# Optimization experiments

Hardware: AMD Instinct MI355X
Metric: run time of the kernel (lower is better)

## Reference

```python
import jax, jax.numpy as jnp
import numpy as np

HEADS = 4
K = 3  # neighborhood kernel size
EPS = 1e-5


def _nbr_idx(dim, k):
    # NATTEN semantics: window start clamped so the full k-window stays in-bounds.
    i = jnp.arange(dim)
    start = jnp.clip(i - k // 2, 0, dim - k)
    return start[:, None] + jnp.arange(k)[None, :]  # [dim, k]


def _gather_windows(t, ix, iy, iz):
    # t: [B, X, Y, Z, n, c] -> [B, X, Y, Z, K^3, n, c]
    t = t[:, ix]                 # [B, X, k, Y, Z, n, c]
    t = t[:, :, :, iy]           # [B, X, k, Y, k, Z, n, c]
    t = t[:, :, :, :, :, iz]     # [B, X, k, Y, k, Z, k, n, c]
    t = t.transpose(0, 1, 3, 5, 2, 4, 6, 7, 8)  # [B,X,Y,Z,k,k,k,n,c]
    B, X, Y, Z = t.shape[0], t.shape[1], t.shape[2], t.shape[3]
    return t.reshape(B, X, Y, Z, K * K * K, HEADS, -1)


def setup_inputs() -> dict:
    key = jax.random.key(0)
    k1, k2, k3 = jax.random.split(key, 3)
    C = 128
    x = jax.random.normal(k1, (1, C, 32, 32, 32), dtype=jnp.float32)
    ln_gamma = jnp.ones((C,), jnp.float32)
    ln_beta = jnp.zeros((C,), jnp.float32)
    qkv_w = jax.random.normal(k2, (3 * C, C), dtype=jnp.float32) * 0.02
    qkv_b = jnp.zeros((3 * C,), jnp.float32)
    proj_w = jax.random.normal(k3, (C, C), dtype=jnp.float32) * 0.02
    proj_b = jnp.zeros((C,), jnp.float32)
    return {"x": x, "ln_gamma": ln_gamma, "ln_beta": ln_beta,
            "qkv_w": qkv_w, "qkv_b": qkv_b, "proj_w": proj_w, "proj_b": proj_b}


def reference(x, ln_gamma, ln_beta, qkv_w, qkv_b, proj_w, proj_b):
    B, C, X, Y, Z = x.shape
    hd = C // HEADS
    scale = hd ** -0.5

    # permute to channels-last + LayerNorm over C
    h = x.transpose(0, 2, 3, 4, 1)  # [B,X,Y,Z,C]
    mu = jnp.mean(h, axis=-1, keepdims=True)
    var = jnp.mean(jnp.square(h - mu), axis=-1, keepdims=True)
    h = (h - mu) * jax.lax.rsqrt(var + EPS) * ln_gamma + ln_beta

    # QKV projection
    qkv = h @ qkv_w.T + qkv_b                     # [B,X,Y,Z,3C]
    q, k, v = jnp.split(qkv, 3, axis=-1)
    q = q.reshape(B, X, Y, Z, HEADS, hd)
    k = k.reshape(B, X, Y, Z, HEADS, hd)
    v = v.reshape(B, X, Y, Z, HEADS, hd)

    ix, iy, iz = _nbr_idx(X, K), _nbr_idx(Y, K), _nbr_idx(Z, K)
    k_win = _gather_windows(k, ix, iy, iz)  # [B,X,Y,Z,27,n,hd]
    v_win = _gather_windows(v, ix, iy, iz)

    attn = jnp.einsum('bxyznc,bxyzknc->bxyznk', q * scale, k_win)
    attn = jax.nn.softmax(attn, axis=-1)
    out = jnp.einsum('bxyznk,bxyzknc->bxyznc', attn, v_win)
    out = out.reshape(B, X, Y, Z, C)

    out = out @ proj_w.T + proj_b                 # output projection
    return out.transpose(0, 4, 1, 2, 3) + x      # residual, channels-first
```

## Files before the change

### kernel.cpp

```cpp
#include <hip/hip_runtime.h>

#define N_VOX 32768
#define CCH 128
#define EPSV 1e-5f

typedef __attribute__((ext_vector_type(8))) short bfrag;
typedef __attribute__((ext_vector_type(4))) float ffrag;

__device__ __forceinline__ float bf2f(unsigned short u) {
    union { unsigned int i; float f; } c; c.i = ((unsigned int)u) << 16; return c.f;
}
__device__ __forceinline__ float bf2f_lo(unsigned int u) {
    union { unsigned int i; float f; } c; c.i = u << 16; return c.f;
}
__device__ __forceinline__ float bf2f_hi(unsigned int u) {
    union { unsigned int i; float f; } c; c.i = u & 0xFFFF0000u; return c.f;
}
__device__ __forceinline__ unsigned short f2bf(float f) {
    union { float f; unsigned int i; } c; c.f = f;
    unsigned int i = c.i;
    return (unsigned short)((i + 0x7FFFu + ((i >> 16) & 1u)) >> 16);
}

__global__ __launch_bounds__(256) void ln_kernel(const float* __restrict__ x,
                                                 const float* __restrict__ gamma,
                                                 const float* __restrict__ beta,
                                                 unsigned short* __restrict__ h) {
    __shared__ float xs[128 * 65];
    __shared__ float g[128], b[128];
    __shared__ float ps[256], pq[256];
    __shared__ float muS[64], rsS[64];
    int t = threadIdx.x;
    int v0 = blockIdx.x * 64;
    if (t < 128) { g[t] = gamma[t]; b[t] = beta[t]; }
    int vv = t & 63, cq = t >> 6;
    for (int cb = 0; cb < 32; cb++) {
        int c = cb * 4 + cq;
        xs[c * 65 + vv] = x[(size_t)c * N_VOX + v0 + vv];
    }
    __syncthreads();
    float s = 0.f, sq = 0.f;
    for (int i = 0; i < 32; i++) {
        float val = xs[(cq * 32 + i) * 65 + vv];
        s += val; sq += val * val;
    }
    ps[t] = s; pq[t] = sq;
    __syncthreads();
    if (t < 64) {
        float S = ps[t] + ps[t + 64] + ps[t + 128] + ps[t + 192];
        float Q = pq[t] + pq[t + 64] + pq[t + 128] + pq[t + 192];
        float mu = S * (1.0f / 128.0f);
        float var = Q * (1.0f / 128.0f) - mu * mu;
        muS[t] = mu; rsS[t] = rsqrtf(var + EPSV);
    }
    __syncthreads();
    int c8 = t & 15;
    for (int pass = 0; pass < 4; pass++) {
        int v = pass * 16 + (t >> 4);
        float mu = muS[v], rs = rsS[v];
        union { unsigned short u[8]; uint4 q; } pk;
        #pragma unroll
        for (int i = 0; i < 8; i++) {
            int c = c8 * 8 + i;
            float val = (xs[c * 65 + v] - mu) * rs * g[c] + b[c];
            pk.u[i] = f2bf(val);
        }
        *(uint4*)&h[(size_t)(v0 + v) * 128 + c8 * 8] = pk.q;
    }
}

__global__ __launch_bounds__(256) void qkv_gemm(const unsigned short* __restrict__ h,
                                                const float* __restrict__ w,
                                                const float* __restrict__ bias,
                                                unsigned short* __restrict__ qkv) {
    __shared__ __align__(16) unsigned short a_s[64 * 136];
    __shared__ __align__(16) unsigned short b_s[64 * 136];
    int t = threadIdx.x;
    int m0 = blockIdx.x * 64, o0 = blockIdx.y * 64;
    {
        int r4 = t >> 4, c8 = t & 15;
        #pragma unroll
        for (int pass = 0; pass < 4; pass++) {
            int r = pass * 16 + r4;
            *(uint4*)&a_s[r * 136 + c8 * 8] =
                *(const uint4*)&h[(size_t)(m0 + r) * 128 + c8 * 8];
            float4 w0 = *(const float4*)&w[(size_t)(o0 + r) * 128 + c8 * 8];
            float4 w1 = *(const float4*)&w[(size_t)(o0 + r) * 128 + c8 * 8 + 4];
            union { unsigned short u[8]; uint4 q; } pk;
            pk.u[0] = f2bf(w0.x); pk.u[1] = f2bf(w0.y);
            pk.u[2] = f2bf(w0.z); pk.u[3] = f2bf(w0.w);
            pk.u[4] = f2bf(w1.x); pk.u[5] = f2bf(w1.y);
            pk.u[6] = f2bf(w1.z); pk.u[7] = f2bf(w1.w);
            *(uint4*)&b_s[r * 136 + c8 * 8] = pk.q;
        }
    }
    __syncthreads();
    int wvi = t >> 6, lane = t & 63, m = lane & 15, quad = lane >> 4;
    ffrag acc[4] = {ffrag{0,0,0,0}, ffrag{0,0,0,0}, ffrag{0,0,0,0}, ffrag{0,0,0,0}};
    #pragma unroll
    for (int kk = 0; kk < 4; kk++) {
        bfrag a = *(bfrag*)&a_s[(wvi * 16 + m) * 136 + kk * 32 + quad * 8];
        #pragma unroll
        for (int nt = 0; nt < 4; nt++) {
            bfrag bb = *(bfrag*)&b_s[(nt * 16 + m) * 136 + kk * 32 + quad * 8];
            acc[nt] = __builtin_amdgcn_mfma_f32_16x16x32_bf16(a, bb, acc[nt], 0, 0, 0);
        }
    }
    #pragma unroll
    for (int nt = 0; nt < 4; nt++) {
        int o = o0 + nt * 16 + m;
        float bs = bias[o];
        int sec = o >> 7;
        int oc = o & 127;
        unsigned short* dst = qkv + (size_t)sec * ((size_t)N_VOX * 128);
        #pragma unroll
        for (int r = 0; r < 4; r++) {
            int vg = m0 + wvi * 16 + quad * 4 + r;
            dst[(size_t)vg * 128 + oc] = f2bf(acc[nt][r] + bs);
        }
    }
}

__global__ __launch_bounds__(256) void attn_kernel(const unsigned int* __restrict__ qb,
                                                   const unsigned int* __restrict__ kb,
                                                   const unsigned int* __restrict__ vb,
                                                   unsigned int* __restrict__ ob) {
    int t = threadIdx.x;
    int wave = t >> 6, lane = t & 63;
    int v = blockIdx.x * 4 + wave;
    int z = v & 31, y = (v >> 5) & 31, x = v >> 10;
    int sx = min(max(x - 1, 0), 29);
    int sy = min(max(y - 1, 0), 29);
    int sz = min(max(z - 1, 0), 29);
    int base = (sx << 10) + (sy << 5) + sz;
    const float scale = 0.17677669529663687f;
    unsigned int qpk = qb[(size_t)v * 64 + lane];
    float q0 = bf2f_lo(qpk) * scale;
    float q1 = bf2f_hi(qpk) * scale;
    float s[27];
    unsigned int vpk[27];
    #pragma unroll
    for (int j = 0; j < 27; j++) {
        int jx = j / 9, jy = (j % 9) / 3, jz = j % 3;
        int vj = base + (jx << 10) + (jy << 5) + jz;
        size_t idx = (size_t)vj * 64 + lane;
        unsigned int kpk = kb[idx];
        vpk[j] = vb[idx];
        float p = q0 * bf2f_lo(kpk) + q1 * bf2f_hi(kpk);
        p += __shfl_xor(p, 8);
        p += __shfl_xor(p, 4);
        p += __shfl_xor(p, 2);
        p += __shfl_xor(p, 1);
        s[j] = p;
    }
    float mx = s[0];
    #pragma unroll
    for (int j = 1; j < 27; j++) mx = fmaxf(mx, s[j]);
    float sum = 0.f;
    #pragma unroll
    for (int j = 0; j < 27; j++) { s[j] = __expf(s[j] - mx); sum += s[j]; }
    float inv = 1.0f / sum;
    float o0 = 0.f, o1 = 0.f;
    #pragma unroll
    for (int j = 0; j < 27; j++) {
        o0 += s[j] * bf2f_lo(vpk[j]);
        o1 += s[j] * bf2f_hi(vpk[j]);
    }
    unsigned int opk = ((unsigned int)f2bf(o0 * inv)) | (((unsigned int)f2bf(o1 * inv)) << 16);
    ob[(size_t)v * 64 + lane] = opk;
}

__global__ __launch_bounds__(256) void proj_gemm(const unsigned short* __restrict__ a,
                                                 const float* __restrict__ w,
                                                 const float* __restrict__ bias,
                                                 const float* __restrict__ xres,
                                                 float* __restrict__ out) {
    __shared__ __align__(16) unsigned short a_s[64 * 136];
    __shared__ __align__(16) unsigned short b_s[64 * 136];
    int t = threadIdx.x;
    int m0 = blockIdx.x * 64, o0 = blockIdx.y * 64;
    {
        int r4 = t >> 4, c8 = t & 15;
        #pragma unroll
        for (int pass = 0; pass < 4; pass++) {
            int r = pass * 16 + r4;
            *(uint4*)&a_s[r * 136 + c8 * 8] =
                *(const uint4*)&a[(size_t)(m0 + r) * 128 + c8 * 8];
            float4 w0 = *(const float4*)&w[(size_t)(o0 + r) * 128 + c8 * 8];
            float4 w1 = *(const float4*)&w[(size_t)(o0 + r) * 128 + c8 * 8 + 4];
            union { unsigned short u[8]; uint4 q; } pk;
            pk.u[0] = f2bf(w0.x); pk.u[1] = f2bf(w0.y);
            pk.u[2] = f2bf(w0.z); pk.u[3] = f2bf(w0.w);
            pk.u[4] = f2bf(w1.x); pk.u[5] = f2bf(w1.y);
            pk.u[6] = f2bf(w1.z); pk.u[7] = f2bf(w1.w);
            *(uint4*)&b_s[r * 136 + c8 * 8] = pk.q;
        }
    }
    __syncthreads();
    int wvi = t >> 6, lane = t & 63, m = lane & 15, quad = lane >> 4;
    ffrag acc[4] = {ffrag{0,0,0,0}, ffrag{0,0,0,0}, ffrag{0,0,0,0}, ffrag{0,0,0,0}};
    #pragma unroll
    for (int kk = 0; kk < 4; kk++) {
        bfrag av = *(bfrag*)&a_s[(wvi * 16 + m) * 136 + kk * 32 + quad * 8];
        #pragma unroll
        for (int nt = 0; nt < 4; nt++) {
            bfrag bb = *(bfrag*)&b_s[(nt * 16 + m) * 136 + kk * 32 + quad * 8];
            acc[nt] = __builtin_amdgcn_mfma_f32_16x16x32_bf16(av, bb, acc[nt], 0, 0, 0);
        }
    }
    #pragma unroll
    for (int nt = 0; nt < 4; nt++) {
        int o = o0 + nt * 16 + m;
        float bs = bias[o];
        int vg = m0 + wvi * 16 + quad * 4;
        float4 r = *(const float4*)&xres[(size_t)o * N_VOX + vg];
        float4 ov;
        ov.x = acc[nt][0] + bs + r.x;
        ov.y = acc[nt][1] + bs + r.y;
        ov.z = acc[nt][2] + bs + r.z;
        ov.w = acc[nt][3] + bs + r.w;
        *(float4*)&out[(size_t)o * N_VOX + vg] = ov;
    }
}

extern "C" void kernel_launch(void* const* d_in, const int* in_sizes, int n_in,
                              void* d_out, int out_size, void* d_ws, size_t ws_size,
                              hipStream_t stream) {
    const float* x      = (const float*)d_in[0];
    const float* gamma  = (const float*)d_in[1];
    const float* beta   = (const float*)d_in[2];
    const float* qkv_w  = (const float*)d_in[3];
    const float* qkv_b  = (const float*)d_in[4];
    const float* proj_w = (const float*)d_in[5];
    const float* proj_b = (const float*)d_in[6];
    float* out = (float*)d_out;

    unsigned short* h    = (unsigned short*)d_ws;
    unsigned short* qkv  = (unsigned short*)((char*)d_ws + (8u << 20));
    unsigned short* attn = h;

    hipLaunchKernelGGL(ln_kernel, dim3(512), dim3(256), 0, stream, x, gamma, beta, h);
    hipLaunchKernelGGL(qkv_gemm, dim3(512, 6), dim3(256), 0, stream, h, qkv_w, qkv_b, qkv);
    const unsigned short* qb = qkv;
    const unsigned short* kb = qkv + (size_t)N_VOX * 128;
    const unsigned short* vb = qkv + (size_t)2 * N_VOX * 128;
    hipLaunchKernelGGL(attn_kernel, dim3(8192), dim3(256), 0, stream,
                       (const unsigned int*)qb, (const unsigned int*)kb,
                       (const unsigned int*)vb, (unsigned int*)attn);
    hipLaunchKernelGGL(proj_gemm, dim3(512, 2), dim3(256), 0, stream, attn, proj_w, proj_b, x, out);
}
```

Before: 139.0 us.

## Fuse LayerNorm into QKV GEMM and pre-convert weights to bf16 once

LayerNorm output is now written directly into shared memory and reused by a single block that loops over all six QKV output tiles. This removes the global round trip of the normalized activations and the separate LN launch. A small kernel converts qkv_w and proj_w to bf16 once per call, so GEMM blocks no longer repeat the fp32-to-bf16 weight conversion. proj_gemm also loops over both output tiles per block, reusing the activation tile, and the attention output is written in place over q. The trade-off is far fewer blocks (512 instead of 3072 for QKV), more serialized work per block, and extra barriers, which may lower latency hiding.

```diff
diff --git a/kernel.cpp b/kernel.cpp
--- a/kernel.cpp
+++ b/kernel.cpp
@@ -7,9 +7,6 @@
 typedef __attribute__((ext_vector_type(8))) short bfrag;
 typedef __attribute__((ext_vector_type(4))) float ffrag;
 
-__device__ __forceinline__ float bf2f(unsigned short u) {
-    union { unsigned int i; float f; } c; c.i = ((unsigned int)u) << 16; return c.f;
-}
 __device__ __forceinline__ float bf2f_lo(unsigned int u) {
     union { unsigned int i; float f; } c; c.i = u << 16; return c.f;
 }
@@ -22,14 +19,39 @@
     return (unsigned short)((i + 0x7FFFu + ((i >> 16) & 1u)) >> 16);
 }
 
-__global__ __launch_bounds__(256) void ln_kernel(const float* __restrict__ x,
-                                                 const float* __restrict__ gamma,
-                                                 const float* __restrict__ beta,
-                                                 unsigned short* __restrict__ h) {
-    __shared__ float xs[128 * 65];
+__global__ __launch_bounds__(256) void convw_kernel(const float* __restrict__ qkv_w,
+                                                    const float* __restrict__ proj_w,
+                                                    unsigned short* __restrict__ wq,
+                                                    unsigned short* __restrict__ wp) {
+    int i = (blockIdx.x * 256 + threadIdx.x) * 4;
+    if (i < 384 * 128) {
+        float4 v = *(const float4*)&qkv_w[i];
+        ushort4 pk;
+        pk.x = f2bf(v.x); pk.y = f2bf(v.y); pk.z = f2bf(v.z); pk.w = f2bf(v.w);
+        *(ushort4*)&wq[i] = pk;
+    } else {
+        int j = i - 384 * 128;
+        float4 v = *(const float4*)&proj_w[j];
+        ushort4 pk;
+        pk.x = f2bf(v.x); pk.y = f2bf(v.y); pk.z = f2bf(v.z); pk.w = f2bf(v.w);
+        *(ushort4*)&wp[j] = pk;
+    }
+}
+
+__global__ __launch_bounds__(256) void ln_qkv_kernel(const float* __restrict__ x,
+                                                     const float* __restrict__ gamma,
+                                                     const float* __restrict__ beta,
+                                                     const unsigned short* __restrict__ wq,
+                                                     const float* __restrict__ bias,
+                                                     unsigned short* __restrict__ qkv) {
+    __shared__ __align__(16) unsigned short a_s[64 * 136];
+    __shared__ __align__(16) char pool[128 * 65 * 4];
     __shared__ float g[128], b[128];
     __shared__ float ps[256], pq[256];
     __shared__ float muS[64], rsS[64];
+    float* xs = (float*)pool;
+    unsigned short* b_s = (unsigned short*)pool;
+
     int t = threadIdx.x;
     int v0 = blockIdx.x * 64;
     if (t < 128) { g[t] = gamma[t]; b[t] = beta[t]; }
@@ -54,70 +76,60 @@
         muS[t] = mu; rsS[t] = rsqrtf(var + EPSV);
     }
     __syncthreads();
-    int c8 = t & 15;
-    for (int pass = 0; pass < 4; pass++) {
-        int v = pass * 16 + (t >> 4);
-        float mu = muS[v], rs = rsS[v];
-        union { unsigned short u[8]; uint4 q; } pk;
-        #pragma unroll
-        for (int i = 0; i < 8; i++) {
-            int c = c8 * 8 + i;
-            float val = (xs[c * 65 + v] - mu) * rs * g[c] + b[c];
-            pk.u[i] = f2bf(val);
-        }
-        *(uint4*)&h[(size_t)(v0 + v) * 128 + c8 * 8] = pk.q;
-    }
-}
-
-__global__ __launch_bounds__(256) void qkv_gemm(const unsigned short* __restrict__ h,
-                                                const float* __restrict__ w,
-                                                const float* __restrict__ bias,
-                                                unsigned short* __restrict__ qkv) {
-    __shared__ __align__(16) unsigned short a_s[64 * 136];
-    __shared__ __align__(16) unsigned short b_s[64 * 136];
-    int t = threadIdx.x;
-    int m0 = blockIdx.x * 64, o0 = blockIdx.y * 64;
     {
-        int r4 = t >> 4, c8 = t & 15;
+        int c8 = t & 15;
+        #pragma unroll
+        for (int pass = 0; pass < 4; pass++) {
+            int v = pass * 16 + (t >> 4);
+            float mu = muS[v], rs = rsS[v];
+            union { unsigned short u[8]; uint4 q; } pk;
+            #pragma unroll
+            for (int i = 0; i < 8; i++) {
+                int c = c8 * 8 + i;
+                float val = (xs[c * 65 + v] - mu) * rs * g[c] + b[c];
+                pk.u[i] = f2bf(val);
+            }
+            *(uint4*)&a_s[v * 136 + c8 * 8] = pk.q;
+        }
+    }
+    __syncthreads();
+
+    int wvi = t >> 6, lane = t & 63, m = lane & 15, quad = lane >> 4;
+    int r4 = t >> 4, c8 = t & 15;
+
+    for (int ot = 0; ot < 6; ot++) {
+        int o0 = ot * 64;
         #pragma unroll
         for (int pass = 0; pass < 4; pass++) {
             int r = pass * 16 + r4;
-            *(uint4*)&a_s[r * 136 + c8 * 8] =
-                *(const uint4*)&h[(size_t)(m0 + r) * 128 + c8 * 8];
-            float4 w0 = *(const float4*)&w[(size_t)(o0 + r) * 128 + c8 * 8];
-            float4 w1 = *(const float4*)&w[(size_t)(o0 + r) * 128 + c8 * 8 + 4];
-            union { unsigned short u[8]; uint4 q; } pk;
-            pk.u[0] = f2bf(w0.x); pk.u[1] = f2bf(w0.y);
-            pk.u[2] = f2bf(w0.z); pk.u[3] = f2bf(w0.w);
-            pk.u[4] = f2bf(w1.x); pk.u[5] = f2bf(w1.y);
-            pk.u[6] = f2bf(w1.z); pk.u[7] = f2bf(w1.w);
-            *(uint4*)&b_s[r * 136 + c8 * 8] = pk.q;
-        }
-    }
-    __syncthreads();
-    int wvi = t >> 6, lane = t & 63, m = lane & 15, quad = lane >> 4;
-    ffrag acc[4] = {ffrag{0,0,0,0}, ffrag{0,0,0,0}, ffrag{0,0,0,0}, ffrag{0,0,0,0}};
-    #pragma unroll
-    for (int kk = 0; kk < 4; kk++) {
-        bfrag a = *(bfrag*)&a_s[(wvi * 16 + m) * 136 + kk * 32 + quad * 8];
+            *(uint4*)&b_s[r * 136 + c8 * 8] =
+                *(const uint4*)&wq[(size_t)(o0 + r) * 128 + c8 * 8];
+        }
+        __syncthreads();
+        ffrag acc[4] = {ffrag{0,0,0,0}, ffrag{0,0,0,0}, ffrag{0,0,0,0}, ffrag{0,0,0,0}};
+        #pragma unroll
+        for (int kk = 0; kk < 4; kk++) {
+            bfrag a = *(bfrag*)&a_s[(wvi * 16 + m) * 136 + kk * 32 + quad * 8];
+            #pragma unroll
+            for (int nt = 0; nt < 4; nt++) {
+                bfrag bb = *(bfrag*)&b_s[(nt * 16 + m) * 136 + kk * 32 + quad * 8];
+                acc[nt] = __builtin_amdgcn_mfma_f32_16x16x32_bf16(a, bb, acc[nt], 0, 0, 0);
+            }
+        }
         #pragma unroll
         for (int nt = 0; nt < 4; nt++) {
-            bfrag bb = *(bfrag*)&b_s[(nt * 16 + m) * 136 + kk * 32 + quad * 8];
-            acc[nt] = __builtin_amdgcn_mfma_f32_16x16x32_bf16(a, bb, acc[nt], 0, 0, 0);
-        }
-    }
-    #pragma unroll
-    for (int nt = 0; nt < 4; nt++) {
-        int o = o0 + nt * 16 + m;
-        float bs = bias[o];
-        int sec = o >> 7;
-        int oc = o & 127;
-        unsigned short* dst = qkv + (size_t)sec * ((size_t)N_VOX * 128);
-        #pragma unroll
-        for (int r = 0; r < 4; r++) {
-            int vg = m0 + wvi * 16 + quad * 4 + r;
-            dst[(size_t)vg * 128 + oc] = f2bf(acc[nt][r] + bs);
-        }
+            int o = o0 + nt * 16 + m;
+            float bs = bias[o];
+            int sec = o >> 7;
+            int oc = o & 127;
+            unsigned short* dst = qkv + (size_t)sec * ((size_t)N_VOX * 128);
+            #pragma unroll
+            for (int r = 0; r < 4; r++) {
+                int vg = v0 + wvi * 16 + quad * 4 + r;
+                dst[(size_t)vg * 128 + oc] = f2bf(acc[nt][r] + bs);
+            }
+        }
+        __syncthreads();
     }
 }
 
@@ -171,55 +183,56 @@
 }
 
 __global__ __launch_bounds__(256) void proj_gemm(const unsigned short* __restrict__ a,
-                                                 const float* __restrict__ w,
+                                                 const unsigned short* __restrict__ wp,
                                                  const float* __restrict__ bias,
                                                  const float* __restrict__ xres,
                                                  float* __restrict__ out) {
     __shared__ __align__(16) unsigned short a_s[64 * 136];
     __shared__ __align__(16) unsigned short b_s[64 * 136];
     int t = threadIdx.x;
-    int m0 = blockIdx.x * 64, o0 = blockIdx.y * 64;
-    {
-        int r4 = t >> 4, c8 = t & 15;
+    int m0 = blockIdx.x * 64;
+    int r4 = t >> 4, c8 = t & 15;
+    #pragma unroll
+    for (int pass = 0; pass < 4; pass++) {
+        int r = pass * 16 + r4;
+        *(uint4*)&a_s[r * 136 + c8 * 8] =
+            *(const uint4*)&a[(size_t)(m0 + r) * 128 + c8 * 8];
+    }
+    int wvi = t >> 6, lane = t & 63, m = lane & 15, quad = lane >> 4;
+
+    for (int ot = 0; ot < 2; ot++) {
+        int o0 = ot * 64;
         #pragma unroll
         for (int pass = 0; pass < 4; pass++) {
             int r = pass * 16 + r4;
-            *(uint4*)&a_s[r * 136 + c8 * 8] =
-                *(const uint4*)&a[(size_t)(m0 + r) * 128 + c8 * 8];
-            float4 w0 = *(const float4*)&w[(size_t)(o0 + r) * 128 + c8 * 8];
-            float4 w1 = *(const float4*)&w[(size_t)(o0 + r) * 128 + c8 * 8 + 4];
-            union { unsigned short u[8]; uint4 q; } pk;
-            pk.u[0] = f2bf(w0.x); pk.u[1] = f2bf(w0.y);
-            pk.u[2] = f2bf(w0.z); pk.u[3] = f2bf(w0.w);
-            pk.u[4] = f2bf(w1.x); pk.u[5] = f2bf(w1.y);
-            pk.u[6] = f2bf(w1.z); pk.u[7] = f2bf(w1.w);
-            *(uint4*)&b_s[r * 136 + c8 * 8] = pk.q;
-        }
-    }
-    __syncthreads();
-    int wvi = t >> 6, lane = t & 63, m = lane & 15, quad = lane >> 4;
-    ffrag acc[4] = {ffrag{0,0,0,0}, ffrag{0,0,0,0}, ffrag{0,0,0,0}, ffrag{0,0,0,0}};
-    #pragma unroll
-    for (int kk = 0; kk < 4; kk++) {
-        bfrag av = *(bfrag*)&a_s[(wvi * 16 + m) * 136 + kk * 32 + quad * 8];
+            *(uint4*)&b_s[r * 136 + c8 * 8] =
+                *(const uint4*)&wp[(size_t)(o0 + r) * 128 + c8 * 8];
+        }
+        __syncthreads();
+        ffrag acc[4] = {ffrag{0,0,0,0}, ffrag{0,0,0,0}, ffrag{0,0,0,0}, ffrag{0,0,0,0}};
+        #pragma unroll
+        for (int kk = 0; kk < 4; kk++) {
+            bfrag av = *(bfrag*)&a_s[(wvi * 16 + m) * 136 + kk * 32 + quad * 8];
+            #pragma unroll
+            for (int nt = 0; nt < 4; nt++) {
+                bfrag bb = *(bfrag*)&b_s[(nt * 16 + m) * 136 + kk * 32 + quad * 8];
+                acc[nt] = __builtin_amdgcn_mfma_f32_16x16x32_bf16(av, bb, acc[nt], 0, 0, 0);
+            }
+        }
         #pragma unroll
         for (int nt = 0; nt < 4; nt++) {
-            bfrag bb = *(bfrag*)&b_s[(nt * 16 + m) * 136 + kk * 32 + quad * 8];
-            acc[nt] = __builtin_amdgcn_mfma_f32_16x16x32_bf16(av, bb, acc[nt], 0, 0, 0);
-        }
-    }
-    #pragma unroll
-    for (int nt = 0; nt < 4; nt++) {
-        int o = o0 + nt * 16 + m;
-        float bs = bias[o];
-        int vg = m0 + wvi * 16 + quad * 4;
-        float4 r = *(const float4*)&xres[(size_t)o * N_VOX + vg];
-        float4 ov;
-        ov.x = acc[nt][0] + bs + r.x;
-        ov.y = acc[nt][1] + bs + r.y;
-        ov.z = acc[nt][2] + bs + r.z;
-        ov.w = acc[nt][3] + bs + r.w;
-        *(float4*)&out[(size_t)o * N_VOX + vg] = ov;
+            int o = o0 + nt * 16 + m;
+            float bs = bias[o];
+            int vg = m0 + wvi * 16 + quad * 4;
+            float4 r = *(const float4*)&xres[(size_t)o * N_VOX + vg];
+            float4 ov;
+            ov.x = acc[nt][0] + bs + r.x;
+            ov.y = acc[nt][1] + bs + r.y;
+            ov.z = acc[nt][2] + bs + r.z;
+            ov.w = acc[nt][3] + bs + r.w;
+            *(float4*)&out[(size_t)o * N_VOX + vg] = ov;
+        }
+        __syncthreads();
     }
 }
 
@@ -235,17 +248,18 @@
     const float* proj_b = (const float*)d_in[6];
     float* out = (float*)d_out;
 
-    unsigned short* h    = (unsigned short*)d_ws;
+    unsigned short* wq   = (unsigned short*)d_ws;
+    unsigned short* wp   = wq + 384 * 128;
     unsigned short* qkv  = (unsigned short*)((char*)d_ws + (8u << 20));
-    unsigned short* attn = h;
-
-    hipLaunchKernelGGL(ln_kernel, dim3(512), dim3(256), 0, stream, x, gamma, beta, h);
-    hipLaunchKernelGGL(qkv_gemm, dim3(512, 6), dim3(256), 0, stream, h, qkv_w, qkv_b, qkv);
-    const unsigned short* qb = qkv;
-    const unsigned short* kb = qkv + (size_t)N_VOX * 128;
-    const unsigned short* vb = qkv + (size_t)2 * N_VOX * 128;
+    unsigned short* qb   = qkv;
+    unsigned short* kb   = qkv + (size_t)N_VOX * 128;
+    unsigned short* vb   = qkv + (size_t)2 * N_VOX * 128;
+    unsigned short* attn = qb;
+
+    hipLaunchKernelGGL(convw_kernel, dim3(64), dim3(256), 0, stream, qkv_w, proj_w, wq, wp);
+    hipLaunchKernelGGL(ln_qkv_kernel, dim3(512), dim3(256), 0, stream, x, gamma, beta, wq, qkv_b, qkv);
     hipLaunchKernelGGL(attn_kernel, dim3(8192), dim3(256), 0, stream,
                        (const unsigned int*)qb, (const unsigned int*)kb,
                        (const unsigned int*)vb, (unsigned int*)attn);
-    hipLaunchKernelGGL(proj_gemm, dim3(512, 2), dim3(256), 0, stream, attn, proj_w, proj_b, x, out);
-}
+    hipLaunchKernelGGL(proj_gemm, dim3(512), dim3(256), 0, stream, attn, wp, proj_b, x, out);
+}
```

Result: no change. 139.7 us (+0.6%).

## Fuse LayerNorm into QKV GEMM and attention into output projection

Applied to the files above, without the earlier changes.

Merges the LayerNorm and QKV projection into one kernel that keeps normalized activations in shared memory, and merges neighborhood attention with the output projection so attention results never go to global memory. Weights are now read straight from global memory and converted to bf16 inside the MFMA loop rather than staged through shared memory. Each attention wave now handles two voxels at a time to expose more memory-level parallelism. In exchange, weight loads and conversions are repeated per wave, and register pressure rises from the doubled per-voxel arrays.

```diff
diff --git a/kernel.cpp b/kernel.cpp
--- a/kernel.cpp
+++ b/kernel.cpp
@@ -1,15 +1,11 @@
 #include <hip/hip_runtime.h>
 
 #define N_VOX 32768
-#define CCH 128
 #define EPSV 1e-5f
 
 typedef __attribute__((ext_vector_type(8))) short bfrag;
 typedef __attribute__((ext_vector_type(4))) float ffrag;
 
-__device__ __forceinline__ float bf2f(unsigned short u) {
-    union { unsigned int i; float f; } c; c.i = ((unsigned int)u) << 16; return c.f;
-}
 __device__ __forceinline__ float bf2f_lo(unsigned int u) {
     union { unsigned int i; float f; } c; c.i = u << 16; return c.f;
 }
@@ -21,205 +17,197 @@
     unsigned int i = c.i;
     return (unsigned short)((i + 0x7FFFu + ((i >> 16) & 1u)) >> 16);
 }
-
-__global__ __launch_bounds__(256) void ln_kernel(const float* __restrict__ x,
-                                                 const float* __restrict__ gamma,
-                                                 const float* __restrict__ beta,
-                                                 unsigned short* __restrict__ h) {
-    __shared__ float xs[128 * 65];
-    __shared__ float g[128], b[128];
+__device__ __forceinline__ bfrag pack8(float4 a, float4 b) {
+    bfrag r;
+    r[0] = (short)f2bf(a.x); r[1] = (short)f2bf(a.y);
+    r[2] = (short)f2bf(a.z); r[3] = (short)f2bf(a.w);
+    r[4] = (short)f2bf(b.x); r[5] = (short)f2bf(b.y);
+    r[6] = (short)f2bf(b.z); r[7] = (short)f2bf(b.w);
+    return r;
+}
+
+__global__ __launch_bounds__(256) void ln_qkv_kernel(const float* __restrict__ x,
+                                                     const float* __restrict__ gamma,
+                                                     const float* __restrict__ beta,
+                                                     const float* __restrict__ w,
+                                                     const float* __restrict__ bias,
+                                                     unsigned short* __restrict__ qkv) {
+    __shared__ __align__(16) unsigned short a_s[32 * 136];
+    __shared__ float xs[128 * 33];
+    __shared__ float g[128], bta[128];
     __shared__ float ps[256], pq[256];
-    __shared__ float muS[64], rsS[64];
+    __shared__ float muS[32], rsS[32];
+
     int t = threadIdx.x;
-    int v0 = blockIdx.x * 64;
-    if (t < 128) { g[t] = gamma[t]; b[t] = beta[t]; }
-    int vv = t & 63, cq = t >> 6;
-    for (int cb = 0; cb < 32; cb++) {
-        int c = cb * 4 + cq;
-        xs[c * 65 + vv] = x[(size_t)c * N_VOX + v0 + vv];
+    int v0 = blockIdx.x * 32;
+    if (t < 128) { g[t] = gamma[t]; bta[t] = beta[t]; }
+    int vv = t & 31, cq = t >> 5;
+    #pragma unroll
+    for (int cb = 0; cb < 16; cb++) {
+        int c = cb * 8 + cq;
+        xs[c * 33 + vv] = x[(size_t)c * N_VOX + v0 + vv];
     }
     __syncthreads();
     float s = 0.f, sq = 0.f;
-    for (int i = 0; i < 32; i++) {
-        float val = xs[(cq * 32 + i) * 65 + vv];
+    #pragma unroll
+    for (int i = 0; i < 16; i++) {
+        float val = xs[(cq * 16 + i) * 33 + vv];
         s += val; sq += val * val;
     }
     ps[t] = s; pq[t] = sq;
     __syncthreads();
-    if (t < 64) {
-        float S = ps[t] + ps[t + 64] + ps[t + 128] + ps[t + 192];
-        float Q = pq[t] + pq[t + 64] + pq[t + 128] + pq[t + 192];
+    if (t < 32) {
+        float S = 0.f, Q = 0.f;
+        #pragma unroll
+        for (int k = 0; k < 8; k++) { S += ps[t + k * 32]; Q += pq[t + k * 32]; }
         float mu = S * (1.0f / 128.0f);
         float var = Q * (1.0f / 128.0f) - mu * mu;
         muS[t] = mu; rsS[t] = rsqrtf(var + EPSV);
     }
     __syncthreads();
-    int c8 = t & 15;
-    for (int pass = 0; pass < 4; pass++) {
-        int v = pass * 16 + (t >> 4);
-        float mu = muS[v], rs = rsS[v];
-        union { unsigned short u[8]; uint4 q; } pk;
-        #pragma unroll
-        for (int i = 0; i < 8; i++) {
-            int c = c8 * 8 + i;
-            float val = (xs[c * 65 + v] - mu) * rs * g[c] + b[c];
-            pk.u[i] = f2bf(val);
-        }
-        *(uint4*)&h[(size_t)(v0 + v) * 128 + c8 * 8] = pk.q;
-    }
-}
-
-__global__ __launch_bounds__(256) void qkv_gemm(const unsigned short* __restrict__ h,
-                                                const float* __restrict__ w,
-                                                const float* __restrict__ bias,
-                                                unsigned short* __restrict__ qkv) {
-    __shared__ __align__(16) unsigned short a_s[64 * 136];
-    __shared__ __align__(16) unsigned short b_s[64 * 136];
-    int t = threadIdx.x;
-    int m0 = blockIdx.x * 64, o0 = blockIdx.y * 64;
     {
-        int r4 = t >> 4, c8 = t & 15;
-        #pragma unroll
-        for (int pass = 0; pass < 4; pass++) {
-            int r = pass * 16 + r4;
-            *(uint4*)&a_s[r * 136 + c8 * 8] =
-                *(const uint4*)&h[(size_t)(m0 + r) * 128 + c8 * 8];
-            float4 w0 = *(const float4*)&w[(size_t)(o0 + r) * 128 + c8 * 8];
-            float4 w1 = *(const float4*)&w[(size_t)(o0 + r) * 128 + c8 * 8 + 4];
+        int c8 = t & 15;
+        #pragma unroll
+        for (int pass = 0; pass < 2; pass++) {
+            int v = pass * 16 + (t >> 4);
+            float mu = muS[v], rs = rsS[v];
             union { unsigned short u[8]; uint4 q; } pk;
-            pk.u[0] = f2bf(w0.x); pk.u[1] = f2bf(w0.y);
-            pk.u[2] = f2bf(w0.z); pk.u[3] = f2bf(w0.w);
-            pk.u[4] = f2bf(w1.x); pk.u[5] = f2bf(w1.y);
-            pk.u[6] = f2bf(w1.z); pk.u[7] = f2bf(w1.w);
-            *(uint4*)&b_s[r * 136 + c8 * 8] = pk.q;
-        }
-    }
-    __syncthreads();
-    int wvi = t >> 6, lane = t & 63, m = lane & 15, quad = lane >> 4;
-    ffrag acc[4] = {ffrag{0,0,0,0}, ffrag{0,0,0,0}, ffrag{0,0,0,0}, ffrag{0,0,0,0}};
-    #pragma unroll
-    for (int kk = 0; kk < 4; kk++) {
-        bfrag a = *(bfrag*)&a_s[(wvi * 16 + m) * 136 + kk * 32 + quad * 8];
+            #pragma unroll
+            for (int i = 0; i < 8; i++) {
+                int c = c8 * 8 + i;
+                float val = (xs[c * 33 + v] - mu) * rs * g[c] + bta[c];
+                pk.u[i] = f2bf(val);
+            }
+            *(uint4*)&a_s[v * 136 + c8 * 8] = pk.q;
+        }
+    }
+    __syncthreads();
+
+    int wave = t >> 6, lane = t & 63, m = lane & 15, quad = lane >> 4;
+    int msub = wave & 1;
+    int sgrp = wave >> 1;
+
+    for (int it = 0; it < 3; it++) {
+        int o0 = (sgrp * 3 + it) * 64;
+        ffrag acc[4] = {ffrag{0,0,0,0}, ffrag{0,0,0,0}, ffrag{0,0,0,0}, ffrag{0,0,0,0}};
+        #pragma unroll
+        for (int kk = 0; kk < 4; kk++) {
+            bfrag a = *(bfrag*)&a_s[(msub * 16 + m) * 136 + kk * 32 + quad * 8];
+            #pragma unroll
+            for (int nt = 0; nt < 4; nt++) {
+                const float* wr = &w[(size_t)(o0 + nt * 16 + m) * 128 + kk * 32 + quad * 8];
+                bfrag bb = pack8(*(const float4*)wr, *(const float4*)(wr + 4));
+                acc[nt] = __builtin_amdgcn_mfma_f32_16x16x32_bf16(a, bb, acc[nt], 0, 0, 0);
+            }
+        }
         #pragma unroll
         for (int nt = 0; nt < 4; nt++) {
-            bfrag bb = *(bfrag*)&b_s[(nt * 16 + m) * 136 + kk * 32 + quad * 8];
-            acc[nt] = __builtin_amdgcn_mfma_f32_16x16x32_bf16(a, bb, acc[nt], 0, 0, 0);
-        }
-    }
-    #pragma unroll
-    for (int nt = 0; nt < 4; nt++) {
-        int o = o0 + nt * 16 + m;
-        float bs = bias[o];
-        int sec = o >> 7;
-        int oc = o & 127;
-        unsigned short* dst = qkv + (size_t)sec * ((size_t)N_VOX * 128);
-        #pragma unroll
-        for (int r = 0; r < 4; r++) {
-            int vg = m0 + wvi * 16 + quad * 4 + r;
-            dst[(size_t)vg * 128 + oc] = f2bf(acc[nt][r] + bs);
-        }
-    }
-}
-
-__global__ __launch_bounds__(256) void attn_kernel(const unsigned int* __restrict__ qb,
-                                                   const unsigned int* __restrict__ kb,
-                                                   const unsigned int* __restrict__ vb,
-                                                   unsigned int* __restrict__ ob) {
+            int o = o0 + nt * 16 + m;
+            float bs = bias[o];
+            int sec = o >> 7;
+            int oc = o & 127;
+            unsigned short* dst = qkv + (size_t)sec * ((size_t)N_VOX * 128);
+            #pragma unroll
+            for (int r = 0; r < 4; r++) {
+                int vg = v0 + msub * 16 + quad * 4 + r;
+                dst[(size_t)vg * 128 + oc] = f2bf(acc[nt][r] + bs);
+            }
+        }
+    }
+}
+
+__global__ __launch_bounds__(256) void attn_proj_kernel(const unsigned int* __restrict__ qb,
+                                                        const unsigned int* __restrict__ kb,
+                                                        const unsigned int* __restrict__ vb,
+                                                        const float* __restrict__ w,
+                                                        const float* __restrict__ bias,
+                                                        const float* __restrict__ xres,
+                                                        float* __restrict__ out) {
+    __shared__ __align__(16) unsigned short att_s[16 * 136];
     int t = threadIdx.x;
     int wave = t >> 6, lane = t & 63;
-    int v = blockIdx.x * 4 + wave;
-    int z = v & 31, y = (v >> 5) & 31, x = v >> 10;
-    int sx = min(max(x - 1, 0), 29);
-    int sy = min(max(y - 1, 0), 29);
-    int sz = min(max(z - 1, 0), 29);
-    int base = (sx << 10) + (sy << 5) + sz;
+    int v0 = blockIdx.x * 16;
     const float scale = 0.17677669529663687f;
-    unsigned int qpk = qb[(size_t)v * 64 + lane];
-    float q0 = bf2f_lo(qpk) * scale;
-    float q1 = bf2f_hi(qpk) * scale;
-    float s[27];
-    unsigned int vpk[27];
-    #pragma unroll
-    for (int j = 0; j < 27; j++) {
-        int jx = j / 9, jy = (j % 9) / 3, jz = j % 3;
-        int vj = base + (jx << 10) + (jy << 5) + jz;
-        size_t idx = (size_t)vj * 64 + lane;
-        unsigned int kpk = kb[idx];
-        vpk[j] = vb[idx];
-        float p = q0 * bf2f_lo(kpk) + q1 * bf2f_hi(kpk);
-        p += __shfl_xor(p, 8);
-        p += __shfl_xor(p, 4);
-        p += __shfl_xor(p, 2);
-        p += __shfl_xor(p, 1);
-        s[j] = p;
-    }
-    float mx = s[0];
-    #pragma unroll
-    for (int j = 1; j < 27; j++) mx = fmaxf(mx, s[j]);
-    float sum = 0.f;
-    #pragma unroll
-    for (int j = 0; j < 27; j++) { s[j] = __expf(s[j] - mx); sum += s[j]; }
-    float inv = 1.0f / sum;
-    float o0 = 0.f, o1 = 0.f;
-    #pragma unroll
-    for (int j = 0; j < 27; j++) {
-        o0 += s[j] * bf2f_lo(vpk[j]);
-        o1 += s[j] * bf2f_hi(vpk[j]);
-    }
-    unsigned int opk = ((unsigned int)f2bf(o0 * inv)) | (((unsigned int)f2bf(o1 * inv)) << 16);
-    ob[(size_t)v * 64 + lane] = opk;
-}
-
-__global__ __launch_bounds__(256) void proj_gemm(const unsigned short* __restrict__ a,
-                                                 const float* __restrict__ w,
-                                                 const float* __restrict__ bias,
-                                                 const float* __restrict__ xres,
-                                                 float* __restrict__ out) {
-    __shared__ __align__(16) unsigned short a_s[64 * 136];
-    __shared__ __align__(16) unsigned short b_s[64 * 136];
-    int t = threadIdx.x;
-    int m0 = blockIdx.x * 64, o0 = blockIdx.y * 64;
-    {
-        int r4 = t >> 4, c8 = t & 15;
-        #pragma unroll
-        for (int pass = 0; pass < 4; pass++) {
-            int r = pass * 16 + r4;
-            *(uint4*)&a_s[r * 136 + c8 * 8] =
-                *(const uint4*)&a[(size_t)(m0 + r) * 128 + c8 * 8];
-            float4 w0 = *(const float4*)&w[(size_t)(o0 + r) * 128 + c8 * 8];
-            float4 w1 = *(const float4*)&w[(size_t)(o0 + r) * 128 + c8 * 8 + 4];
-            union { unsigned short u[8]; uint4 q; } pk;
-            pk.u[0] = f2bf(w0.x); pk.u[1] = f2bf(w0.y);
-            pk.u[2] = f2bf(w0.z); pk.u[3] = f2bf(w0.w);
-            pk.u[4] = f2bf(w1.x); pk.u[5] = f2bf(w1.y);
-            pk.u[6] = f2bf(w1.z); pk.u[7] = f2bf(w1.w);
-            *(uint4*)&b_s[r * 136 + c8 * 8] = pk.q;
-        }
-    }
-    __syncthreads();
-    int wvi = t >> 6, lane = t & 63, m = lane & 15, quad = lane >> 4;
-    ffrag acc[4] = {ffrag{0,0,0,0}, ffrag{0,0,0,0}, ffrag{0,0,0,0}, ffrag{0,0,0,0}};
+
+    for (int p = 0; p < 2; p++) {
+        int vA = v0 + wave * 4 + p * 2;
+        int vB = vA + 1;
+        int zA = vA & 31, yA = (vA >> 5) & 31, xA = vA >> 10;
+        int baseA = (min(max(xA - 1, 0), 29) << 10) + (min(max(yA - 1, 0), 29) << 5)
+                  + min(max(zA - 1, 0), 29);
+        int zB = vB & 31;
+        int baseB = (min(max(xA - 1, 0), 29) << 10) + (min(max(yA - 1, 0), 29) << 5)
+                  + min(max(zB - 1, 0), 29);
+        unsigned int qpA = qb[(size_t)vA * 64 + lane];
+        unsigned int qpB = qb[(size_t)vB * 64 + lane];
+        float qA0 = bf2f_lo(qpA) * scale, qA1 = bf2f_hi(qpA) * scale;
+        float qB0 = bf2f_lo(qpB) * scale, qB1 = bf2f_hi(qpB) * scale;
+        float sA[27], sB[27];
+        unsigned int vpA[27], vpB[27];
+        #pragma unroll
+        for (int j = 0; j < 27; j++) {
+            int off = ((j / 9) << 10) + (((j % 9) / 3) << 5) + (j % 3);
+            size_t iA = (size_t)(baseA + off) * 64 + lane;
+            size_t iB = (size_t)(baseB + off) * 64 + lane;
+            unsigned int kA = kb[iA], kB = kb[iB];
+            vpA[j] = vb[iA]; vpB[j] = vb[iB];
+            float pA = qA0 * bf2f_lo(kA) + qA1 * bf2f_hi(kA);
+            float pB = qB0 * bf2f_lo(kB) + qB1 * bf2f_hi(kB);
+            pA += __shfl_xor(pA, 8);  pB += __shfl_xor(pB, 8);
+            pA += __shfl_xor(pA, 4);  pB += __shfl_xor(pB, 4);
+            pA += __shfl_xor(pA, 2);  pB += __shfl_xor(pB, 2);
+            pA += __shfl_xor(pA, 1);  pB += __shfl_xor(pB, 1);
+            sA[j] = pA; sB[j] = pB;
+        }
+        float mA = sA[0], mB = sB[0];
+        #pragma unroll
+        for (int j = 1; j < 27; j++) { mA = fmaxf(mA, sA[j]); mB = fmaxf(mB, sB[j]); }
+        float suA = 0.f, suB = 0.f;
+        #pragma unroll
+        for (int j = 0; j < 27; j++) {
+            sA[j] = __expf(sA[j] - mA); suA += sA[j];
+            sB[j] = __expf(sB[j] - mB); suB += sB[j];
+        }
+        float ivA = 1.0f / suA, ivB = 1.0f / suB;
+        float oA0 = 0.f, oA1 = 0.f, oB0 = 0.f, oB1 = 0.f;
+        #pragma unroll
+        for (int j = 0; j < 27; j++) {
+            oA0 += sA[j] * bf2f_lo(vpA[j]); oA1 += sA[j] * bf2f_hi(vpA[j]);
+            oB0 += sB[j] * bf2f_lo(vpB[j]); oB1 += sB[j] * bf2f_hi(vpB[j]);
+        }
+        unsigned int pkA = ((unsigned int)f2bf(oA0 * ivA)) | (((unsigned int)f2bf(oA1 * ivA)) << 16);
+        unsigned int pkB = ((unsigned int)f2bf(oB0 * ivB)) | (((unsigned int)f2bf(oB1 * ivB)) << 16);
+        int vloc = wave * 4 + p * 2;
+        *(unsigned int*)&att_s[vloc * 136 + lane * 2] = pkA;
+        *(unsigned int*)&att_s[(vloc + 1) * 136 + lane * 2] = pkB;
+    }
+    __syncthreads();
+
+    int m = lane & 15, quad = lane >> 4;
+    ffrag acc0 = ffrag{0,0,0,0}, acc1 = ffrag{0,0,0,0};
     #pragma unroll
     for (int kk = 0; kk < 4; kk++) {
-        bfrag av = *(bfrag*)&a_s[(wvi * 16 + m) * 136 + kk * 32 + quad * 8];
-        #pragma unroll
-        for (int nt = 0; nt < 4; nt++) {
-            bfrag bb = *(bfrag*)&b_s[(nt * 16 + m) * 136 + kk * 32 + quad * 8];
-            acc[nt] = __builtin_amdgcn_mfma_f32_16x16x32_bf16(av, bb, acc[nt], 0, 0, 0);
-        }
-    }
-    #pragma unroll
-    for (int nt = 0; nt < 4; nt++) {
-        int o = o0 + nt * 16 + m;
-        float bs = bias[o];
-        int vg = m0 + wvi * 16 + quad * 4;
-        float4 r = *(const float4*)&xres[(size_t)o * N_VOX + vg];
+        bfrag a = *(bfrag*)&att_s[m * 136 + kk * 32 + quad * 8];
+        const float* wr0 = &w[(size_t)((wave * 2 + 0) * 16 + m) * 128 + kk * 32 + quad * 8];
+        const float* wr1 = &w[(size_t)((wave * 2 + 1) * 16 + m) * 128 + kk * 32 + quad * 8];
+        bfrag b0 = pack8(*(const float4*)wr0, *(const float4*)(wr0 + 4));
+        bfrag b1 = pack8(*(const float4*)wr1, *(const float4*)(wr1 + 4));
+        acc0 = __builtin_amdgcn_mfma_f32_16x16x32_bf16(a, b0, acc0, 0, 0, 0);
+        acc1 = __builtin_amdgcn_mfma_f32_16x16x32_bf16(a, b1, acc1, 0, 0, 0);
+    }
+    #pragma unroll
+    for (int nt = 0; nt < 2; nt++) {
+        ffrag acc = nt ? acc1 : acc0;
+        int c = (wave * 2 + nt) * 16 + m;
+        float bs = bias[c];
+        int vg = v0 + quad * 4;
+        float4 r = *(const float4*)&xres[(size_t)c * N_VOX + vg];
         float4 ov;
-        ov.x = acc[nt][0] + bs + r.x;
-        ov.y = acc[nt][1] + bs + r.y;
-        ov.z = acc[nt][2] + bs + r.z;
-        ov.w = acc[nt][3] + bs + r.w;
-        *(float4*)&out[(size_t)o * N_VOX + vg] = ov;
+        ov.x = acc[0] + bs + r.x;
+        ov.y = acc[1] + bs + r.y;
+        ov.z = acc[2] + bs + r.z;
+        ov.w = acc[3] + bs + r.w;
+        *(float4*)&out[(size_t)c * N_VOX + vg] = ov;
     }
 }
 
@@ -235,17 +223,14 @@
     const float* proj_b = (const float*)d_in[6];
     float* out = (float*)d_out;
 
-    unsigned short* h    = (unsigned short*)d_ws;
-    unsigned short* qkv  = (unsigned short*)((char*)d_ws + (8u << 20));
-    unsigned short* attn = h;
-
-    hipLaunchKernelGGL(ln_kernel, dim3(512), dim3(256), 0, stream, x, gamma, beta, h);
-    hipLaunchKernelGGL(qkv_gemm, dim3(512, 6), dim3(256), 0, stream, h, qkv_w, qkv_b, qkv);
+    unsigned short* qkv = (unsigned short*)d_ws;
     const unsigned short* qb = qkv;
     const unsigned short* kb = qkv + (size_t)N_VOX * 128;
     const unsigned short* vb = qkv + (size_t)2 * N_VOX * 128;
-    hipLaunchKernelGGL(attn_kernel, dim3(8192), dim3(256), 0, stream,
+
+    hipLaunchKernelGGL(ln_qkv_kernel, dim3(1024), dim3(256), 0, stream,
+                       x, gamma, beta, qkv_w, qkv_b, qkv);
+    hipLaunchKernelGGL(attn_proj_kernel, dim3(2048), dim3(256), 0, stream,
                        (const unsigned int*)qb, (const unsigned int*)kb,
-                       (const unsigned int*)vb, (unsigned int*)attn);
-    hipLaunchKernelGGL(proj_gemm, dim3(512, 2), dim3(256), 0, stream, attn, proj_w, proj_b, x, out);
-}
+                       (const unsigned int*)vb, proj_w, proj_b, x, out);
+}
```

Measured after the change: 204.9 us. +47.5%, slower.
